# Optimization experiments

Hardware: AMD Instinct MI355X
Metric: run time of the kernel (lower is better)

The kernel has to match this reference:

```python
import jax, jax.numpy as jnp
import numpy as np


def _rbf(X1, X2, log_ls):
    # exp(-||x1-x2||^2 / (2*ls^2)) via the squared-norm expansion
    sq1 = jnp.sum(X1 * X1, axis=-1)[:, None]
    sq2 = jnp.sum(X2 * X2, axis=-1)[None, :]
    d2 = jnp.maximum(sq1 + sq2 - 2.0 * (X1 @ X2.T), 0.0)
    ls2 = jnp.exp(2.0 * log_ls)
    return jnp.exp(-d2 / (2.0 * ls2))


def setup_inputs() -> dict:
    key = jax.random.key(0)
    k1, k2, k3 = jax.random.split(key, 3)
    N_way, K_shot, Q_query, D = 16, 32, 4096, 1024
    Zs = jax.random.normal(k1, (N_way * K_shot, D), dtype=jnp.float32)
    Ys = jax.random.randint(k2, (N_way * K_shot, 1), 0, N_way)
    Zq = jax.random.normal(k3, (N_way * Q_query, D), dtype=jnp.float32)
    log_ls = jnp.asarray(0.0, dtype=jnp.float32)
    log_noise = jnp.asarray(-3.0, dtype=jnp.float32)
    return {"Zs": Zs, "Ys": Ys, "Zq": Zq, "log_ls": log_ls,
            "log_noise": log_noise, "N_way": N_way}


def reference(Zs, Ys, Zq, log_ls, log_noise, N_way):
    Nsamp = Zs.shape[0]  # N_way * K_shot
    Y1hot = jax.nn.one_hot(Ys.reshape(-1), N_way, dtype=Zs.dtype)  # [Nsamp, N_way]
    noise = jnp.exp(2.0 * log_noise)
    Kss = _rbf(Zs, Zs, log_ls) + noise * jnp.eye(Nsamp, dtype=Zs.dtype)
    L = jnp.linalg.cholesky(Kss)
    alpha = jax.scipy.linalg.cho_solve((L, True), Y1hot)  # [Nsamp, N_way]
    Kqs = _rbf(Zq, Zs, log_ls)  # [Q, Nsamp]
    f_q = Kqs @ alpha  # [Q, N_way]
    return jax.nn.softmax(f_q, axis=-1)
```

## Files before the change

kernel.cpp:

```cpp
#include <hip/hip_runtime.h>
#include <math.h>

#define NS 512
#define NQ 65536
#define DD 1024
#define NW 16

typedef __attribute__((ext_vector_type(8))) short short8x;
typedef __attribute__((ext_vector_type(4))) float floatx4;

static __device__ __forceinline__ unsigned short bf_trunc(float x) {
  return (unsigned short)(__float_as_uint(x) >> 16);
}
static __device__ __forceinline__ float bf_tof(unsigned short h) {
  return __uint_as_float(((unsigned)h) << 16);
}
static __device__ __forceinline__ unsigned short bf_rne(float x) {
  unsigned u = __float_as_uint(x);
  return (unsigned short)((u + 0x7FFFu + ((u >> 16) & 1u)) >> 16);
}

#define STASH(Hp, Lp, row, k0, v) do {                                      \
    unsigned e_ = (unsigned)((((row) * 32 + (k0)) ^ (((row) & 7) << 3)));   \
    ushort4 h_, l_;                                                         \
    h_.x = bf_trunc((v).x); l_.x = bf_trunc((v).x - bf_tof(h_.x));          \
    h_.y = bf_trunc((v).y); l_.y = bf_trunc((v).y - bf_tof(h_.y));          \
    h_.z = bf_trunc((v).z); l_.z = bf_trunc((v).z - bf_tof(h_.z));          \
    h_.w = bf_trunc((v).w); l_.w = bf_trunc((v).w - bf_tof(h_.w));          \
    *(ushort4*)&Hp[e_] = h_; *(ushort4*)&Lp[e_] = l_;                       \
  } while (0)

__global__ void row_norms_kernel(const float* __restrict__ X, float* __restrict__ out, int nrows) {
  int gw = (int)((blockIdx.x * blockDim.x + threadIdx.x) >> 6);
  int lane = threadIdx.x & 63;
  if (gw >= nrows) return;
  const float* row = X + (size_t)gw * DD;
  float s = 0.f;
  #pragma unroll
  for (int i = 0; i < 4; ++i) {
    float4 v = *(const float4*)(row + 4 * lane + 256 * i);
    s += v.x * v.x + v.y * v.y + v.z * v.z + v.w * v.w;
  }
  #pragma unroll
  for (int off = 32; off; off >>= 1) s += __shfl_xor(s, off);
  if (lane == 0) out[gw] = s;
}

__global__ __launch_bounds__(256) void kss_kernel(const float* __restrict__ Zs,
                                                  const float* __restrict__ sn,
                                                  const float* __restrict__ log_ls,
                                                  const float* __restrict__ log_noise,
                                                  float* __restrict__ K) {
  __shared__ __align__(16) float At[16][68];
  __shared__ __align__(16) float Bt[16][68];
  int tid = threadIdx.x;
  int rb = blockIdx.y * 64, cb = blockIdx.x * 64;
  int tx = tid & 15, ty = tid >> 4;
  int srow = tid & 63, skq = (tid >> 6) << 2;
  float acc[4][4] = {};
  for (int kk = 0; kk < DD; kk += 16) {
    __syncthreads();
    float4 a = *(const float4*)(Zs + (size_t)(rb + srow) * DD + kk + skq);
    float4 b = *(const float4*)(Zs + (size_t)(cb + srow) * DD + kk + skq);
    At[skq + 0][srow] = a.x; At[skq + 1][srow] = a.y; At[skq + 2][srow] = a.z; At[skq + 3][srow] = a.w;
    Bt[skq + 0][srow] = b.x; Bt[skq + 1][srow] = b.y; Bt[skq + 2][srow] = b.z; Bt[skq + 3][srow] = b.w;
    __syncthreads();
    #pragma unroll
    for (int k = 0; k < 16; ++k) {
      float4 av = *(const float4*)&At[k][ty * 4];
      float4 bv = *(const float4*)&Bt[k][tx * 4];
      float aa[4] = {av.x, av.y, av.z, av.w};
      float bb[4] = {bv.x, bv.y, bv.z, bv.w};
      #pragma unroll
      for (int i = 0; i < 4; ++i)
        #pragma unroll
        for (int j = 0; j < 4; ++j)
          acc[i][j] = fmaf(aa[i], bb[j], acc[i][j]);
    }
  }
  float inv2 = 0.5f * expf(-2.f * log_ls[0]);
  float noise = expf(2.f * log_noise[0]);
  #pragma unroll
  for (int i = 0; i < 4; ++i)
    #pragma unroll
    for (int j = 0; j < 4; ++j) {
      int r = rb + ty * 4 + i, c = cb + tx * 4 + j;
      float d2 = fmaxf(sn[r] + sn[c] - 2.f * acc[i][j], 0.f);
      float v = expf(-d2 * inv2);
      if (r == c) v += noise;
      K[(size_t)r * NS + c] = v;
    }
}

__global__ __launch_bounds__(512) void chol_panel(float* __restrict__ K, int j) {
  __shared__ float A[64][65];
  __shared__ float diag[64], idia[64];
  int tid = threadIdx.x;
  for (int i = tid; i < 4096; i += 512) {
    int r = i >> 6, c = i & 63;
    A[r][c] = K[(size_t)(j + r) * NS + j + c];
  }
  __syncthreads();
  for (int c = 0; c < 64; ++c) {
    float d = A[c][c];
    float s = sqrtf(d);
    float inv = 1.f / s;
    if (tid == c) { diag[c] = s; idia[c] = inv; }
    if (tid < 64 && tid > c) A[tid][c] *= inv;
    __syncthreads();
    for (int i = tid; i < 4096; i += 512) {
      int r = i >> 6, k = i & 63;
      if (r > c && k > c) A[r][k] -= A[r][c] * A[k][c];
    }
    __syncthreads();
  }
  for (int i = tid; i < 4096; i += 512) {
    int r = i >> 6, c = i & 63;
    if (c <= r) K[(size_t)(j + r) * NS + j + c] = (c == r) ? diag[r] : A[r][c];
  }
  for (int r0 = j + 64 + tid; r0 < NS; r0 += 512) {
    float x[64];
    #pragma unroll
    for (int c = 0; c < 64; ++c) {
      float v = K[(size_t)r0 * NS + j + c];
      #pragma unroll
      for (int k = 0; k < c; ++k) v -= x[k] * A[c][k];
      x[c] = v * idia[c];
    }
    #pragma unroll
    for (int c = 0; c < 64; ++c) K[(size_t)r0 * NS + j + c] = x[c];
  }
}

__global__ __launch_bounds__(256) void syrk_trailing(float* __restrict__ K, int j) {
  int t0 = j + 64;
  int rbt = t0 + blockIdx.y * 64, cbt = t0 + blockIdx.x * 64;
  if (cbt > rbt) return;
  __shared__ float A[64][69];
  __shared__ float B[64][69];
  int tid = threadIdx.x;
  for (int i = tid; i < 64 * 64; i += 256) {
    int r = i >> 6, k = i & 63;
    A[r][k] = K[(size_t)(rbt + r) * NS + j + k];
    B[r][k] = K[(size_t)(cbt + r) * NS + j + k];
  }
  __syncthreads();
  int tx = tid & 15, ty = tid >> 4;
  float acc[4][4] = {};
  for (int k = 0; k < 64; ++k) {
    float aa[4], bb[4];
    #pragma unroll
    for (int i = 0; i < 4; ++i) aa[i] = A[ty * 4 + i][k];
    #pragma unroll
    for (int i = 0; i < 4; ++i) bb[i] = B[tx * 4 + i][k];
    #pragma unroll
    for (int i = 0; i < 4; ++i)
      #pragma unroll
      for (int jj = 0; jj < 4; ++jj)
        acc[i][jj] = fmaf(aa[i], bb[jj], acc[i][jj]);
  }
  #pragma unroll
  for (int i = 0; i < 4; ++i)
    #pragma unroll
    for (int jj = 0; jj < 4; ++jj)
      K[(size_t)(rbt + ty * 4 + i) * NS + cbt + tx * 4 + jj] -= acc[i][jj];
}

__global__ __launch_bounds__(1024) void cho_solve_kernel(const float* __restrict__ K,
                                                         const int* __restrict__ Ys,
                                                         unsigned short* __restrict__ alpha_t) {
  __shared__ float W[NS][NW];
  __shared__ float P[64][68];
  __shared__ float invd[64];
  const int tid = threadIdx.x;
  const int rr = tid >> 4, nn = tid & 15;
  const int pcol = (tid & 15) * 4;

  for (int i = tid; i < NS * NW; i += 1024)
    W[i >> 4][i & 15] = (Ys[i >> 4] == (i & 15)) ? 1.f : 0.f;

  for (int jb = 0; jb < 8; ++jb) {
    const int j = jb << 6;
    __syncthreads();
    *(float4*)&P[rr][pcol] = *(const float4*)(K + (size_t)(j + rr) * NS + j + pcol);
    __syncthreads();
    if (tid < 64) invd[tid] = 1.f / P[tid][tid];
    __syncthreads();
    if (tid < 64) {
      int n = tid & 15, rq = tid >> 4;
      float w[16];
      #pragma unroll
      for (int i = 0; i < 16; ++i) w[i] = W[j + rq + 4 * i][n];
      #pragma unroll
      for (int c = 0; c < 64; ++c) {
        float xc = __shfl(w[c >> 2], ((c & 3) << 4) + n) * invd[c];
        if (rq == (c & 3)) w[c >> 2] = xc;
        #pragma unroll
        for (int i = 0; i < 16; ++i) {
          int r = rq + 4 * i;
          if (r > c) w[i] -= P[r][c] * xc;
        }
      }
      #pragma unroll
      for (int i = 0; i < 16; ++i) W[j + rq + 4 * i][n] = w[i];
    }
    __syncthreads();
    for (int r0 = j + 64; r0 < NS; r0 += 64) {
      __syncthreads();
      *(float4*)&P[rr][pcol] = *(const float4*)(K + (size_t)(r0 + rr) * NS + j + pcol);
      __syncthreads();
      float s = W[r0 + rr][nn];
      #pragma unroll
      for (int c = 0; c < 64; c += 4) {
        float4 p = *(const float4*)&P[rr][c];
        s -= p.x * W[j + c + 0][nn] + p.y * W[j + c + 1][nn]
           + p.z * W[j + c + 2][nn] + p.w * W[j + c + 3][nn];
      }
      W[r0 + rr][nn] = s;
    }
  }
  for (int jb = 7; jb >= 0; --jb) {
    const int j = jb << 6;
    __syncthreads();
    *(float4*)&P[rr][pcol] = *(const float4*)(K + (size_t)(j + rr) * NS + j + pcol);
    __syncthreads();
    if (tid < 64) invd[tid] = 1.f / P[tid][tid];
    __syncthreads();
    if (tid < 64) {
      int n = tid & 15, rq = tid >> 4;
      float w[16];
      #pragma unroll
      for (int i = 0; i < 16; ++i) w[i] = W[j + rq + 4 * i][n];
      #pragma unroll
      for (int c = 63; c >= 0; --c) {
        float xc = __shfl(w[c >> 2], ((c & 3) << 4) + n) * invd[c];
        if (rq == (c & 3)) w[c >> 2] = xc;
        #pragma unroll
        for (int i = 0; i < 16; ++i) {
          int r = rq + 4 * i;
          if (r < c) w[i] -= P[c][r] * xc;
        }
      }
      #pragma unroll
      for (int i = 0; i < 16; ++i) W[j + rq + 4 * i][n] = w[i];
    }
    __syncthreads();
    for (int r0 = j - 64; r0 >= 0; r0 -= 64) {
      __syncthreads();
      *(float4*)&P[rr][pcol] = *(const float4*)(K + (size_t)(j + rr) * NS + r0 + pcol);
      __syncthreads();
      float s = W[r0 + rr][nn];
      #pragma unroll
      for (int c = 0; c < 64; ++c)
        s -= P[c][rr] * W[j + c][nn];
      W[r0 + rr][nn] = s;
    }
  }
  __syncthreads();
  for (int i = tid; i < NS * NW; i += 1024)
    alpha_t[(size_t)(i & 15) * NS + (i >> 4)] = bf_rne(W[i >> 4][i & 15]);
}

__global__ __launch_bounds__(512) void fused_v2(const float* __restrict__ Zq,
                                                const float* __restrict__ Zs,
                                                const float* __restrict__ sn,
                                                const unsigned short* __restrict__ alpha_t,
                                                const float* __restrict__ log_ls,
                                                float* __restrict__ out) {
  __shared__ __align__(16) unsigned short LB[32768];
  __shared__ float qnl[128];
  __shared__ float snl[256];
  unsigned short* AhB = LB;
  unsigned short* AlB = LB + 4096;
  unsigned short* BhB = LB + 8192;
  unsigned short* BlB = LB + 16384;
  unsigned short* KqB = LB;

  const int tid = threadIdx.x;
  const int lane = tid & 63;
  const int w = tid >> 6;
  const int wm = w >> 2, wn = w & 3;
  const int l15 = lane & 15, l4 = lane >> 4;
  const int rb = blockIdx.x * 128;
  const float inv2 = 0.5f * __expf(-2.f * log_ls[0]);
  const unsigned swz = (unsigned)((l15 & 7) << 3);

  if (tid < 128) qnl[tid] = 0.f;
  __syncthreads();

  const int qrow0 = tid >> 3;
  const int qk0 = (tid & 7) * 4;
  const int qrow1 = 64 + qrow0;

  floatx4 facc = {0.f, 0.f, 0.f, 0.f};

  for (int cc = 0; cc < NS; cc += 256) {
    if (tid < 256) snl[tid] = sn[cc + tid];
    floatx4 acc[4][4];
    #pragma unroll
    for (int a = 0; a < 4; ++a)
      #pragma unroll
      for (int b = 0; b < 4; ++b) acc[a][b] = (floatx4){0.f, 0.f, 0.f, 0.f};

    float4 pq0 = *(const float4*)(Zq + (size_t)(rb + qrow0) * DD + qk0);
    float4 pq1 = *(const float4*)(Zq + (size_t)(rb + qrow1) * DD + qk0);
    float4 ps[4];
    #pragma unroll
    for (int u = 0; u < 4; ++u) {
      int idx = tid + (u << 9);
      ps[u] = *(const float4*)(Zs + (size_t)(cc + (idx >> 3)) * DD + ((idx & 7) * 4));
    }

    for (int kt = 0; kt < 32; ++kt) {
      STASH(AhB, AlB, qrow0, qk0, pq0);
      STASH(AhB, AlB, qrow1, qk0, pq1);
      #pragma unroll
      for (int u = 0; u < 4; ++u) {
        int idx = tid + (u << 9);
        int srow = idx >> 3, sk0 = (idx & 7) * 4;
        STASH(BhB, BlB, srow, sk0, ps[u]);
      }
      if (cc == 0) {
        float s0 = pq0.x * pq0.x + pq0.y * pq0.y + pq0.z * pq0.z + pq0.w * pq0.w;
        float s1 = pq1.x * pq1.x + pq1.y * pq1.y + pq1.z * pq1.z + pq1.w * pq1.w;
        #pragma unroll
        for (int d = 1; d < 8; d <<= 1) { s0 += __shfl_xor(s0, d); s1 += __shfl_xor(s1, d); }
        if ((tid & 7) == 0) { qnl[qrow0] += s0; qnl[qrow1] += s1; }
      }
      __syncthreads();
      if (kt < 31) {
        int kk2 = (kt + 1) << 5;
        pq0 = *(const float4*)(Zq + (size_t)(rb + qrow0) * DD + kk2 + qk0);
        pq1 = *(const float4*)(Zq + (size_t)(rb + qrow1) * DD + kk2 + qk0);
        #pragma unroll
        for (int u = 0; u < 4; ++u) {
          int idx = tid + (u << 9);
          ps[u] = *(const float4*)(Zs + (size_t)(cc + (idx >> 3)) * DD + kk2 + ((idx & 7) * 4));
        }
      }
      short8x ah[4], al[4], bh[4], bl[4];
      #pragma unroll
      for (int mi = 0; mi < 4; ++mi) {
        unsigned e = (unsigned)((wm * 64 + mi * 16 + l15) * 32 + 8 * l4) ^ swz;
        ah[mi] = *(const short8x*)&AhB[e];
        al[mi] = *(const short8x*)&AlB[e];
      }
      #pragma unroll
      for (int ni = 0; ni < 4; ++ni) {
        unsigned e = (unsigned)((wn * 64 + ni * 16 + l15) * 32 + 8 * l4) ^ swz;
        bh[ni] = *(const short8x*)&BhB[e];
        bl[ni] = *(const short8x*)&BlB[e];
      }
      #pragma unroll
      for (int mi = 0; mi < 4; ++mi)
        #pragma unroll
        for (int ni = 0; ni < 4; ++ni) {
          acc[mi][ni] = __builtin_amdgcn_mfma_f32_16x16x32_bf16(ah[mi], bh[ni], acc[mi][ni], 0, 0, 0);
          acc[mi][ni] = __builtin_amdgcn_mfma_f32_16x16x32_bf16(ah[mi], bl[ni], acc[mi][ni], 0, 0, 0);
          acc[mi][ni] = __builtin_amdgcn_mfma_f32_16x16x32_bf16(al[mi], bh[ni], acc[mi][ni], 0, 0, 0);
        }
      __syncthreads();
    }

    short8x bfr[8];
    #pragma unroll
    for (int s = 0; s < 8; ++s)
      bfr[s] = *(const short8x*)(alpha_t + ((size_t)l15 * NS + cc + 32 * s + 8 * l4));

    #pragma unroll
    for (int mi = 0; mi < 4; ++mi)
      #pragma unroll
      for (int rr = 0; rr < 4; ++rr) {
        int row_l = wm * 64 + mi * 16 + l4 * 4 + rr;
        float qv = qnl[row_l];
        unsigned sw = (unsigned)((row_l & 7) << 3);
        #pragma unroll
        for (int ni = 0; ni < 4; ++ni) {
          int col = wn * 64 + ni * 16 + l15;
          float d2 = fmaxf(qv + snl[col] - 2.f * acc[mi][ni][rr], 0.f);
          float kq = __expf(-d2 * inv2);
          KqB[(unsigned)(row_l * 256 + col) ^ sw] = bf_rne(kq);
        }
      }
    __syncthreads();
    #pragma unroll
    for (int s = 0; s < 8; ++s) {
      unsigned e = (unsigned)((w * 16 + l15) * 256 + 32 * s + 8 * l4) ^ swz;
      short8x ak = *(const short8x*)&KqB[e];
      facc = __builtin_amdgcn_mfma_f32_16x16x32_bf16(ak, bfr[s], facc, 0, 0, 0);
    }
    __syncthreads();
  }

  #pragma unroll
  for (int r = 0; r < 4; ++r) {
    float v = facc[r];
    float m = v;
    #pragma unroll
    for (int d = 1; d < 16; d <<= 1) m = fmaxf(m, __shfl_xor(m, d));
    float e = __expf(v - m);
    float s = e;
    #pragma unroll
    for (int d = 1; d < 16; d <<= 1) s += __shfl_xor(s, d);
    out[(size_t)(rb + w * 16 + l4 * 4 + r) * NW + l15] = e / s;
  }
}

extern "C" void kernel_launch(void* const* d_in, const int* in_sizes, int n_in,
                              void* d_out, int out_size, void* d_ws, size_t ws_size,
                              hipStream_t stream) {
  (void)in_sizes; (void)n_in; (void)out_size; (void)ws_size;
  const float* Zs = (const float*)d_in[0];
  const int*   Ys = (const int*)d_in[1];
  const float* Zq = (const float*)d_in[2];
  const float* log_ls = (const float*)d_in[3];
  const float* log_noise = (const float*)d_in[4];
  float* out = (float*)d_out;

  float* ws = (float*)d_ws;
  float* K  = ws;
  float* sn = ws + (size_t)NS * NS;
  unsigned short* alpha_t = (unsigned short*)(sn + NS);

  row_norms_kernel<<<128, 256, 0, stream>>>(Zs, sn, NS);
  kss_kernel<<<dim3(8, 8), 256, 0, stream>>>(Zs, sn, log_ls, log_noise, K);
  for (int j = 0; j < NS; j += 64) {
    chol_panel<<<1, 512, 0, stream>>>(K, j);
    int rows = NS - j - 64;
    if (rows > 0) {
      int t = rows / 64;
      syrk_trailing<<<dim3(t, t), 256, 0, stream>>>(K, j);
    }
  }
  cho_solve_kernel<<<1, 1024, 0, stream>>>(K, Ys, alpha_t);
  fused_v2<<<NQ / 128, 512, 0, stream>>>(Zq, Zs, sn, alpha_t, log_ls, out);
}
```

Baseline: 1.654 ms.

## Restructure cholesky solve: register-resident RHS, mirrored L, batched panel loads

```diff
diff --git a/kernel.cpp b/kernel.cpp
--- a/kernel.cpp
+++ b/kernel.cpp
@@ -166,99 +166,167 @@
       K[(size_t)(rbt + ty * 4 + i) * NS + cbt + tx * 4 + jj] -= acc[i][jj];
 }
 
-__global__ __launch_bounds__(1024) void cho_solve_kernel(const float* __restrict__ K,
-                                                         const int* __restrict__ Ys,
-                                                         unsigned short* __restrict__ alpha_t) {
-  __shared__ float W[NS][NW];
+__global__ __launch_bounds__(256) void transpose_fill(float* __restrict__ K) {
+  int bx = blockIdx.x, by = blockIdx.y;
+  if (by < bx) return;
+  int rb = by * 64, cb = bx * 64;
+  __shared__ float T[64][65];
+  int tid = threadIdx.x;
+  int rr = tid >> 4, pc = (tid & 15) * 4;
+  #pragma unroll
+  for (int u = 0; u < 4; ++u) {
+    int r = rr + 16 * u;
+    *(float4*)&T[r][pc] = *(const float4*)(K + (size_t)(rb + r) * NS + cb + pc);
+  }
+  __syncthreads();
+  if (by == bx) {
+    #pragma unroll
+    for (int u = 0; u < 4; ++u) {
+      int r = rr + 16 * u;
+      #pragma unroll
+      for (int i = 0; i < 4; ++i) {
+        int c = pc + i;
+        if (c > r) K[(size_t)(rb + r) * NS + cb + c] = T[c][r];
+      }
+    }
+  } else {
+    #pragma unroll
+    for (int u = 0; u < 4; ++u) {
+      int orr = rr + 16 * u;
+      float4 o;
+      o.x = T[pc + 0][orr]; o.y = T[pc + 1][orr];
+      o.z = T[pc + 2][orr]; o.w = T[pc + 3][orr];
+      *(float4*)(K + (size_t)(cb + orr) * NS + rb + pc) = o;
+    }
+  }
+}
+
+__global__ __launch_bounds__(1024) void cho_solve_v2(const float* __restrict__ K,
+                                                     const int* __restrict__ Ys,
+                                                     unsigned short* __restrict__ alpha_t) {
   __shared__ float P[64][68];
+  __shared__ float WsT[16][68];
+  __shared__ float Wblk[64][16];
   __shared__ float invd[64];
   const int tid = threadIdx.x;
-  const int rr = tid >> 4, nn = tid & 15;
-  const int pcol = (tid & 15) * 4;
-
-  for (int i = tid; i < NS * NW; i += 1024)
-    W[i >> 4][i & 15] = (Ys[i >> 4] == (i & 15)) ? 1.f : 0.f;
+  const int rs = tid >> 4, nn = tid & 15;
+  const int pc = nn * 4;
+
+  float w[8];
+  #pragma unroll
+  for (int k = 0; k < 8; ++k) w[k] = (Ys[rs + 64 * k] == nn) ? 1.f : 0.f;
 
   for (int jb = 0; jb < 8; ++jb) {
     const int j = jb << 6;
     __syncthreads();
-    *(float4*)&P[rr][pcol] = *(const float4*)(K + (size_t)(j + rr) * NS + j + pcol);
-    __syncthreads();
-    if (tid < 64) invd[tid] = 1.f / P[tid][tid];
+    #pragma unroll
+    for (int k = 0; k < 8; ++k) if (k == jb) Wblk[rs][nn] = w[k];
+    *(floatx4*)&P[rs][pc] = *(const floatx4*)(K + (size_t)(j + rs) * NS + j + pc);
     __syncthreads();
     if (tid < 64) {
-      int n = tid & 15, rq = tid >> 4;
-      float w[16];
-      #pragma unroll
-      for (int i = 0; i < 16; ++i) w[i] = W[j + rq + 4 * i][n];
-      #pragma unroll
-      for (int c = 0; c < 64; ++c) {
-        float xc = __shfl(w[c >> 2], ((c & 3) << 4) + n) * invd[c];
-        if (rq == (c & 3)) w[c >> 2] = xc;
-        #pragma unroll
-        for (int i = 0; i < 16; ++i) {
-          int r = rq + 4 * i;
-          if (r > c) w[i] -= P[r][c] * xc;
-        }
-      }
-      #pragma unroll
-      for (int i = 0; i < 16; ++i) W[j + rq + 4 * i][n] = w[i];
-    }
-    __syncthreads();
-    for (int r0 = j + 64; r0 < NS; r0 += 64) {
-      __syncthreads();
-      *(float4*)&P[rr][pcol] = *(const float4*)(K + (size_t)(r0 + rr) * NS + j + pcol);
-      __syncthreads();
-      float s = W[r0 + rr][nn];
-      #pragma unroll
-      for (int c = 0; c < 64; c += 4) {
-        float4 p = *(const float4*)&P[rr][c];
-        s -= p.x * W[j + c + 0][nn] + p.y * W[j + c + 1][nn]
-           + p.z * W[j + c + 2][nn] + p.w * W[j + c + 3][nn];
-      }
-      W[r0 + rr][nn] = s;
-    }
-  }
+      const int n = tid & 15, rq = tid >> 4;
+      invd[tid] = 1.f / P[tid][tid];
+      float w16[16];
+      #pragma unroll
+      for (int i = 0; i < 16; ++i) w16[i] = Wblk[rq + 4 * i][n];
+      #pragma unroll
+      for (int g = 0; g < 16; ++g) {
+        floatx4 p[16];
+        #pragma unroll
+        for (int i = 0; i < 16; ++i) p[i] = *(const floatx4*)&P[rq + 4 * i][4 * g];
+        #pragma unroll
+        for (int cj = 0; cj < 4; ++cj) {
+          const int c = 4 * g + cj;
+          float xc = __shfl(w16[c >> 2], ((c & 3) << 4) + n) * invd[c];
+          if (rq == (c & 3)) w16[c >> 2] = xc;
+          #pragma unroll
+          for (int i = 0; i < 16; ++i) {
+            int r = rq + 4 * i;
+            if (r > c) w16[i] -= p[i][cj] * xc;
+          }
+        }
+      }
+      #pragma unroll
+      for (int i = 0; i < 16; ++i) WsT[n][rq + 4 * i] = w16[i];
+    }
+    __syncthreads();
+    #pragma unroll
+    for (int k = 0; k < 8; ++k) if (k == jb) w[k] = WsT[nn][rs];
+    floatx4 wsr[16];
+    #pragma unroll
+    for (int g = 0; g < 16; ++g) wsr[g] = *(const floatx4*)&WsT[nn][4 * g];
+    #pragma unroll
+    for (int k = 0; k < 8; ++k) {
+      if (k > jb) {
+        const float* lrow = K + (size_t)(rs + 64 * k) * NS + j;
+        float s = w[k];
+        #pragma unroll
+        for (int g = 0; g < 16; ++g) {
+          floatx4 lv = *(const floatx4*)(lrow + 4 * g);
+          s -= lv.x * wsr[g].x + lv.y * wsr[g].y + lv.z * wsr[g].z + lv.w * wsr[g].w;
+        }
+        w[k] = s;
+      }
+    }
+  }
+
   for (int jb = 7; jb >= 0; --jb) {
     const int j = jb << 6;
     __syncthreads();
-    *(float4*)&P[rr][pcol] = *(const float4*)(K + (size_t)(j + rr) * NS + j + pcol);
-    __syncthreads();
-    if (tid < 64) invd[tid] = 1.f / P[tid][tid];
+    #pragma unroll
+    for (int k = 0; k < 8; ++k) if (k == jb) Wblk[rs][nn] = w[k];
+    *(floatx4*)&P[rs][pc] = *(const floatx4*)(K + (size_t)(j + rs) * NS + j + pc);
     __syncthreads();
     if (tid < 64) {
-      int n = tid & 15, rq = tid >> 4;
-      float w[16];
-      #pragma unroll
-      for (int i = 0; i < 16; ++i) w[i] = W[j + rq + 4 * i][n];
-      #pragma unroll
-      for (int c = 63; c >= 0; --c) {
-        float xc = __shfl(w[c >> 2], ((c & 3) << 4) + n) * invd[c];
-        if (rq == (c & 3)) w[c >> 2] = xc;
-        #pragma unroll
-        for (int i = 0; i < 16; ++i) {
-          int r = rq + 4 * i;
-          if (r < c) w[i] -= P[c][r] * xc;
-        }
-      }
-      #pragma unroll
-      for (int i = 0; i < 16; ++i) W[j + rq + 4 * i][n] = w[i];
-    }
-    __syncthreads();
-    for (int r0 = j - 64; r0 >= 0; r0 -= 64) {
-      __syncthreads();
-      *(float4*)&P[rr][pcol] = *(const float4*)(K + (size_t)(j + rr) * NS + r0 + pcol);
-      __syncthreads();
-      float s = W[r0 + rr][nn];
-      #pragma unroll
-      for (int c = 0; c < 64; ++c)
-        s -= P[c][rr] * W[j + c][nn];
-      W[r0 + rr][nn] = s;
-    }
-  }
-  __syncthreads();
-  for (int i = tid; i < NS * NW; i += 1024)
-    alpha_t[(size_t)(i & 15) * NS + (i >> 4)] = bf_rne(W[i >> 4][i & 15]);
+      const int n = tid & 15, rq = tid >> 4;
+      invd[tid] = 1.f / P[tid][tid];
+      float w16[16];
+      #pragma unroll
+      for (int i = 0; i < 16; ++i) w16[i] = Wblk[rq + 4 * i][n];
+      #pragma unroll
+      for (int g = 15; g >= 0; --g) {
+        floatx4 p[16];
+        #pragma unroll
+        for (int i = 0; i < 16; ++i) p[i] = *(const floatx4*)&P[rq + 4 * i][4 * g];
+        #pragma unroll
+        for (int cj = 3; cj >= 0; --cj) {
+          const int c = 4 * g + cj;
+          float xc = __shfl(w16[c >> 2], ((c & 3) << 4) + n) * invd[c];
+          if (rq == (c & 3)) w16[c >> 2] = xc;
+          #pragma unroll
+          for (int i = 0; i < 16; ++i) {
+            int r = rq + 4 * i;
+            if (r < c) w16[i] -= p[i][cj] * xc;
+          }
+        }
+      }
+      #pragma unroll
+      for (int i = 0; i < 16; ++i) WsT[n][rq + 4 * i] = w16[i];
+    }
+    __syncthreads();
+    #pragma unroll
+    for (int k = 0; k < 8; ++k) if (k == jb) w[k] = WsT[nn][rs];
+    floatx4 wsr[16];
+    #pragma unroll
+    for (int g = 0; g < 16; ++g) wsr[g] = *(const floatx4*)&WsT[nn][4 * g];
+    #pragma unroll
+    for (int k = 0; k < 8; ++k) {
+      if (k < jb) {
+        const float* lrow = K + (size_t)(rs + 64 * k) * NS + j;
+        float s = w[k];
+        #pragma unroll
+        for (int g = 0; g < 16; ++g) {
+          floatx4 lv = *(const floatx4*)(lrow + 4 * g);
+          s -= lv.x * wsr[g].x + lv.y * wsr[g].y + lv.z * wsr[g].z + lv.w * wsr[g].w;
+        }
+        w[k] = s;
+      }
+    }
+  }
+
+  #pragma unroll
+  for (int k = 0; k < 8; ++k)
+    alpha_t[(size_t)nn * NS + rs + 64 * k] = bf_rne(w[k]);
 }
 
 __global__ __launch_bounds__(512) void fused_v2(const float* __restrict__ Zq,
@@ -432,6 +500,7 @@
       syrk_trailing<<<dim3(t, t), 256, 0, stream>>>(K, j);
     }
   }
-  cho_solve_kernel<<<1, 1024, 0, stream>>>(K, Ys, alpha_t);
+  transpose_fill<<<dim3(8, 8), 256, 0, stream>>>(K);
+  cho_solve_v2<<<1, 1024, 0, stream>>>(K, Ys, alpha_t);
   fused_v2<<<NQ / 128, 512, 0, stream>>>(Zq, Zs, sn, alpha_t, log_ls, out);
 }
```

After: 1.404 ms. -15.1%, faster.
